# Kernel tuning notes

Measured on AMD Instinct MI355X. Metric: run time of the kernel, lower is better.

## Reference

```python
import jax, jax.numpy as jnp
import numpy as np

# FP4 E2M1 lookup: low 3 bits -> magnitude {0,.5,1,1.5,2,3,4,6}, bit 3 -> sign
FP4_LUT = jnp.array([0.0, 0.5, 1.0, 1.5, 2.0, 3.0, 4.0, 6.0,
                     -0.0, -0.5, -1.0, -1.5, -2.0, -3.0, -4.0, -6.0], dtype=jnp.float32)


def _dequant(packed_i32, scales, group_size):
    """packed_i32: [K/8, N] (8 FP4 nibbles per word along K); scales: [K/group_size, N] fp16.
    Returns dense [K, N] float32 weight."""
    p = packed_i32.astype(jnp.uint32)
    shifts = (jnp.arange(8, dtype=jnp.uint32) * jnp.uint32(4))
    nib = ((p[:, None, :] >> shifts[None, :, None]) & jnp.uint32(0xF)).astype(jnp.int32)  # [K/8,8,N]
    K = p.shape[0] * 8
    vals = FP4_LUT[nib.reshape(K, p.shape[1])]  # [K, N] f32
    g = jnp.arange(K) // group_size
    return vals * scales.astype(jnp.float32)[g]


def setup_inputs() -> dict:
    key = jax.random.key(0)
    k1, k2, k3, k4, k5 = jax.random.split(key, 5)
    B, H, I, G = 32, 4096, 2048, 128
    x = (jax.random.normal(k1, (B, H), dtype=jnp.float32) * 0.5).astype(jnp.float16)
    gate_up_packed = jax.random.bits(k2, (H // 8, 2 * I), dtype=jnp.uint32).astype(jnp.int32)
    down_packed = jax.random.bits(k3, (I // 8, H), dtype=jnp.uint32).astype(jnp.int32)
    gate_up_scales = (jax.random.uniform(k4, (H // G, 2 * I), minval=0.005, maxval=0.02)).astype(jnp.float16)
    down_scales = (jax.random.uniform(k5, (I // G, H), minval=0.005, maxval=0.02)).astype(jnp.float16)
    return {"x": x, "gate_up_packed": gate_up_packed, "gate_up_scales": gate_up_scales,
            "down_packed": down_packed, "down_scales": down_scales, "group_size": G}


def reference(x, gate_up_packed, gate_up_scales, down_packed, down_scales, group_size):
    w_gu = _dequant(gate_up_packed, gate_up_scales, group_size)   # [H, 2I]
    h = jnp.einsum('bh,hn->bn', x.astype(jnp.float32), w_gu)      # [B, 2I]
    inter = h.shape[1] // 2
    act = jax.nn.silu(h[:, :inter]) * h[:, inter:]                # SwiGLU
    w_d = _dequant(down_packed, down_scales, group_size)          # [I, H]
    out = jnp.einsum('bi,ih->bh', act, w_d)
    return out.astype(jnp.float16)
```

## Files before the change

kernel.cpp:

```cpp
#include <hip/hip_runtime.h>
#include <cstdint>

typedef float f32x4 __attribute__((ext_vector_type(4)));

constexpr int Bv = 32;
constexpr int Hv = 4096;
constexpr int Iv = 2048;
constexpr int N1 = 4096;

__device__ __forceinline__ long dec8(uint32_t w) {
  uint32_t lo = w & 0x07070707u;
  uint32_t hi = (w >> 4) & 0x07070707u;
  uint32_t me = __builtin_amdgcn_perm(0x4C484440u, 0x3C383000u, lo);
  uint32_t mo = __builtin_amdgcn_perm(0x4C484440u, 0x3C383000u, hi);
  uint32_t e  = me | ((w & 0x08080808u) << 4);
  uint32_t o  = mo | (w & 0x80808080u);
  uint32_t d0 = __builtin_amdgcn_perm(o, e, 0x05010400u);
  uint32_t d1 = __builtin_amdgcn_perm(o, e, 0x07030602u);
  return (long)(((uint64_t)d1 << 32) | d0);
}

__global__ __launch_bounds__(256) void k_prep(const float* __restrict__ x,
                                              uint32_t* __restrict__ xh,
                                              uint32_t* __restrict__ xl) {
  const int t = blockIdx.x * 256 + threadIdx.x;
  const float* p = x + t * 8;
  f32x4 v0 = *(const f32x4*)p;
  f32x4 v1 = *(const f32x4*)(p + 4);
  float f[8] = {v0[0], v0[1], v0[2], v0[3], v1[0], v1[1], v1[2], v1[3]};
  uint32_t h0 = 0, h1 = 0;
  h0 = __builtin_amdgcn_cvt_pk_fp8_f32(f[0], f[1], h0, false);
  h0 = __builtin_amdgcn_cvt_pk_fp8_f32(f[2], f[3], h0, true);
  h1 = __builtin_amdgcn_cvt_pk_fp8_f32(f[4], f[5], h1, false);
  h1 = __builtin_amdgcn_cvt_pk_fp8_f32(f[6], f[7], h1, true);
  float r[8];
  r[0] = f[0] - __builtin_amdgcn_cvt_f32_fp8(h0, 0);
  r[1] = f[1] - __builtin_amdgcn_cvt_f32_fp8(h0, 1);
  r[2] = f[2] - __builtin_amdgcn_cvt_f32_fp8(h0, 2);
  r[3] = f[3] - __builtin_amdgcn_cvt_f32_fp8(h0, 3);
  r[4] = f[4] - __builtin_amdgcn_cvt_f32_fp8(h1, 0);
  r[5] = f[5] - __builtin_amdgcn_cvt_f32_fp8(h1, 1);
  r[6] = f[6] - __builtin_amdgcn_cvt_f32_fp8(h1, 2);
  r[7] = f[7] - __builtin_amdgcn_cvt_f32_fp8(h1, 3);
  uint32_t l0 = 0, l1 = 0;
  l0 = __builtin_amdgcn_cvt_pk_fp8_f32(r[0], r[1], l0, false);
  l0 = __builtin_amdgcn_cvt_pk_fp8_f32(r[2], r[3], l0, true);
  l1 = __builtin_amdgcn_cvt_pk_fp8_f32(r[4], r[5], l1, false);
  l1 = __builtin_amdgcn_cvt_pk_fp8_f32(r[6], r[7], l1, true);
  xh[t*2] = h0; xh[t*2+1] = h1;
  xl[t*2] = l0; xl[t*2+1] = l1;
}

__global__ __launch_bounds__(1024, 4) void k_gateup(
    const uint8_t* __restrict__ xh, const uint8_t* __restrict__ xl,
    const uint32_t* __restrict__ wp, const float* __restrict__ sc,
    float* __restrict__ hp) {
  __shared__ float lds[16 * 1024];
  const int nt = blockIdx.x >> 1;
  const int kh = blockIdx.x & 1;
  const int wid = threadIdx.x >> 6, lane = threadIdx.x & 63;
  const int q = lane >> 4, r = lane & 15;
  const int n0 = nt * 32;
  const int nA = n0 + r, nB = n0 + 16 + r;

  const int koff = kh * 2048 + wid * 128 + q * 8;
  const uint8_t* pa0h = xh + r * Hv + koff;
  const uint8_t* pa0l = xl + r * Hv + koff;
  const uint8_t* pa1h = xh + (r + 16) * Hv + koff;
  const uint8_t* pa1l = xl + (r + 16) * Hv + koff;
  const uint32_t* pbA = wp + (size_t)(kh * 256 + wid * 16 + q) * N1 + nA;
  const uint32_t* pbB = pbA + 16;

  f32x4 t00 = {0,0,0,0}, t01 = {0,0,0,0}, t10 = {0,0,0,0}, t11 = {0,0,0,0};
  #pragma unroll
  for (int st = 0; st < 4; ++st) {
    long A0h = *(const long*)(pa0h + st * 32);
    long A0l = *(const long*)(pa0l + st * 32);
    long A1h = *(const long*)(pa1h + st * 32);
    long A1l = *(const long*)(pa1l + st * 32);
    long BA = dec8(pbA[(size_t)st * 4 * N1]);
    long BB = dec8(pbB[(size_t)st * 4 * N1]);
    t00 = __builtin_amdgcn_mfma_f32_16x16x32_fp8_fp8(A0h, BA, t00, 0, 0, 0);
    t00 = __builtin_amdgcn_mfma_f32_16x16x32_fp8_fp8(A0l, BA, t00, 0, 0, 0);
    t01 = __builtin_amdgcn_mfma_f32_16x16x32_fp8_fp8(A0h, BB, t01, 0, 0, 0);
    t01 = __builtin_amdgcn_mfma_f32_16x16x32_fp8_fp8(A0l, BB, t01, 0, 0, 0);
    t10 = __builtin_amdgcn_mfma_f32_16x16x32_fp8_fp8(A1h, BA, t10, 0, 0, 0);
    t10 = __builtin_amdgcn_mfma_f32_16x16x32_fp8_fp8(A1l, BA, t10, 0, 0, 0);
    t11 = __builtin_amdgcn_mfma_f32_16x16x32_fp8_fp8(A1h, BB, t11, 0, 0, 0);
    t11 = __builtin_amdgcn_mfma_f32_16x16x32_fp8_fp8(A1l, BB, t11, 0, 0, 0);
  }
  const int g = kh * 16 + wid;
  const float sA = sc[g * N1 + nA];
  const float sB = sc[g * N1 + nB];
  float* my = lds + wid * 1024;
  #pragma unroll
  for (int j = 0; j < 4; ++j) {
    const int rw = q * 4 + j;
    my[rw * 32 + r]             = sA * t00[j];
    my[rw * 32 + 16 + r]        = sB * t01[j];
    my[(16 + rw) * 32 + r]      = sA * t10[j];
    my[(16 + rw) * 32 + 16 + r] = sB * t11[j];
  }
  __syncthreads();
  const int i = threadIdx.x;
  float sum = 0.f;
  #pragma unroll
  for (int w = 0; w < 16; ++w) sum += lds[w * 1024 + i];
  hp[(size_t)kh * (Bv * N1) + (i >> 5) * N1 + n0 + (i & 31)] = sum;
}

__global__ __launch_bounds__(256) void k_swiglu(const float* __restrict__ hp,
                                                uint32_t* __restrict__ ah,
                                                uint32_t* __restrict__ al) {
  const int t = blockIdx.x * 256 + threadIdx.x;
  const int m = t >> 9;
  const int c = (t & 511) * 4;
  constexpr int P = Bv * N1;
  const float* pg = hp + m * N1 + c;
  const float* pu = pg + Iv;
  f32x4 g = *(const f32x4*)pg + *(const f32x4*)(pg + P);
  f32x4 u = *(const f32x4*)pu + *(const f32x4*)(pu + P);
  float a[4];
  #pragma unroll
  for (int j = 0; j < 4; ++j) {
    float gv = g[j];
    float av = gv / (1.0f + __expf(-gv)) * u[j];
    a[j] = fminf(fmaxf(av, -440.0f), 440.0f);
  }
  uint32_t h = 0;
  h = __builtin_amdgcn_cvt_pk_fp8_f32(a[0], a[1], h, false);
  h = __builtin_amdgcn_cvt_pk_fp8_f32(a[2], a[3], h, true);
  float r0 = a[0] - __builtin_amdgcn_cvt_f32_fp8(h, 0);
  float r1 = a[1] - __builtin_amdgcn_cvt_f32_fp8(h, 1);
  float r2 = a[2] - __builtin_amdgcn_cvt_f32_fp8(h, 2);
  float r3 = a[3] - __builtin_amdgcn_cvt_f32_fp8(h, 3);
  uint32_t l = 0;
  l = __builtin_amdgcn_cvt_pk_fp8_f32(r0, r1, l, false);
  l = __builtin_amdgcn_cvt_pk_fp8_f32(r2, r3, l, true);
  ah[t] = h; al[t] = l;
}

__global__ __launch_bounds__(1024, 4) void k_down(
    const uint8_t* __restrict__ ah8, const uint8_t* __restrict__ al8,
    const uint32_t* __restrict__ wp, const float* __restrict__ sc,
    float* __restrict__ out) {
  __shared__ float lds[16 * 512];
  const int n0 = blockIdx.x * 16;
  const int wid = threadIdx.x >> 6, lane = threadIdx.x & 63;
  const int q = lane >> 4, r = lane & 15;
  const int n = n0 + r;

  const int koff = wid * 128 + q * 8;
  const uint8_t* pa0h = ah8 + r * Iv + koff;
  const uint8_t* pa0l = al8 + r * Iv + koff;
  const uint8_t* pa1h = ah8 + (r + 16) * Iv + koff;
  const uint8_t* pa1l = al8 + (r + 16) * Iv + koff;
  const uint32_t* pb = wp + (size_t)(wid * 16 + q) * Hv + n;

  f32x4 t0 = {0,0,0,0}, t1 = {0,0,0,0};
  #pragma unroll
  for (int st = 0; st < 4; ++st) {
    long A0h = *(const long*)(pa0h + st * 32);
    long A0l = *(const long*)(pa0l + st * 32);
    long A1h = *(const long*)(pa1h + st * 32);
    long A1l = *(const long*)(pa1l + st * 32);
    long Bf = dec8(pb[(size_t)st * 4 * Hv]);
    t0 = __builtin_amdgcn_mfma_f32_16x16x32_fp8_fp8(A0h, Bf, t0, 0, 0, 0);
    t0 = __builtin_amdgcn_mfma_f32_16x16x32_fp8_fp8(A0l, Bf, t0, 0, 0, 0);
    t1 = __builtin_amdgcn_mfma_f32_16x16x32_fp8_fp8(A1h, Bf, t1, 0, 0, 0);
    t1 = __builtin_amdgcn_mfma_f32_16x16x32_fp8_fp8(A1l, Bf, t1, 0, 0, 0);
  }
  const float sv = sc[wid * Hv + n];
  float* my = lds + wid * 512;
  #pragma unroll
  for (int j = 0; j < 4; ++j) {
    const int rw = q * 4 + j;
    my[rw * 16 + r]        = sv * t0[j];
    my[(16 + rw) * 16 + r] = sv * t1[j];
  }
  __syncthreads();
  const int i = threadIdx.x;
  if (i < 512) {
    float sum = 0.f;
    #pragma unroll
    for (int w = 0; w < 16; ++w) sum += lds[w * 512 + i];
    out[(i >> 4) * N1 + n0 + (i & 15)] = sum;
  }
}

extern "C" void kernel_launch(void* const* d_in, const int* in_sizes, int n_in,
                              void* d_out, int out_size, void* d_ws, size_t ws_size,
                              hipStream_t stream) {
  const float*    x   = (const float*)d_in[0];
  const uint32_t* gup = (const uint32_t*)d_in[1];
  const float*    gus = (const float*)d_in[2];
  const uint32_t* dnp = (const uint32_t*)d_in[3];
  const float*    dns = (const float*)d_in[4];

  float*    hpart = (float*)d_ws;
  uint8_t*  xh    = (uint8_t*)d_ws + 2*(size_t)Bv*N1*sizeof(float);
  uint8_t*  xl    = xh + Bv*Hv;
  uint8_t*  a8h   = xl + Bv*Hv;
  uint8_t*  a8l   = a8h + Bv*Iv;

  k_prep  <<< 64,  256, 0, stream>>>(x, (uint32_t*)xh, (uint32_t*)xl);
  k_gateup<<<256, 1024, 0, stream>>>(xh, xl, gup, gus, hpart);
  k_swiglu<<< 64,  256, 0, stream>>>(hpart, (uint32_t*)a8h, (uint32_t*)a8l);
  k_down  <<<256, 1024, 0, stream>>>(a8h, a8l, dnp, dns, (float*)d_out);
}
```

Measured before the change: 93.35 us.

## Fuse SwiGLU into gate/up GEMM by pairing gate and up columns per block

Each gate/up block now computes the matching 16 gate and 16 up columns over the full K range. Every wave covers two scale groups and does the SwiGLU activation plus the fp8 hi/lo split directly from the LDS reduction. This removes the separate swiglu kernel, the fp32 partial-sum round trip through global memory and the K-split. In exchange the grid drops from 256 to 128 blocks, each wave does twice the sequential work, and the activation outputs are written as single bytes instead of packed words.

```diff
diff --git a/kernel.cpp b/kernel.cpp
--- a/kernel.cpp
+++ b/kernel.cpp
@@ -51,93 +51,89 @@
   xl[t*2] = l0; xl[t*2+1] = l1;
 }
 
-__global__ __launch_bounds__(1024, 4) void k_gateup(
+__global__ __launch_bounds__(1024, 4) void k_fused(
     const uint8_t* __restrict__ xh, const uint8_t* __restrict__ xl,
     const uint32_t* __restrict__ wp, const float* __restrict__ sc,
-    float* __restrict__ hp) {
-  __shared__ float lds[16 * 1024];
-  const int nt = blockIdx.x >> 1;
-  const int kh = blockIdx.x & 1;
+    uint8_t* __restrict__ a8h, uint8_t* __restrict__ a8l) {
+  __shared__ float ldsg[16 * 512];
+  __shared__ float ldsu[16 * 512];
+  const int c0 = blockIdx.x * 16;
   const int wid = threadIdx.x >> 6, lane = threadIdx.x & 63;
   const int q = lane >> 4, r = lane & 15;
-  const int n0 = nt * 32;
-  const int nA = n0 + r, nB = n0 + 16 + r;
-
-  const int koff = kh * 2048 + wid * 128 + q * 8;
+  const int ng = c0 + r;
+  const int nu = Iv + c0 + r;
+
+  const int koff = wid * 256 + q * 8;
   const uint8_t* pa0h = xh + r * Hv + koff;
   const uint8_t* pa0l = xl + r * Hv + koff;
   const uint8_t* pa1h = xh + (r + 16) * Hv + koff;
   const uint8_t* pa1l = xl + (r + 16) * Hv + koff;
-  const uint32_t* pbA = wp + (size_t)(kh * 256 + wid * 16 + q) * N1 + nA;
-  const uint32_t* pbB = pbA + 16;
-
-  f32x4 t00 = {0,0,0,0}, t01 = {0,0,0,0}, t10 = {0,0,0,0}, t11 = {0,0,0,0};
-  #pragma unroll
-  for (int st = 0; st < 4; ++st) {
-    long A0h = *(const long*)(pa0h + st * 32);
-    long A0l = *(const long*)(pa0l + st * 32);
-    long A1h = *(const long*)(pa1h + st * 32);
-    long A1l = *(const long*)(pa1l + st * 32);
-    long BA = dec8(pbA[(size_t)st * 4 * N1]);
-    long BB = dec8(pbB[(size_t)st * 4 * N1]);
-    t00 = __builtin_amdgcn_mfma_f32_16x16x32_fp8_fp8(A0h, BA, t00, 0, 0, 0);
-    t00 = __builtin_amdgcn_mfma_f32_16x16x32_fp8_fp8(A0l, BA, t00, 0, 0, 0);
-    t01 = __builtin_amdgcn_mfma_f32_16x16x32_fp8_fp8(A0h, BB, t01, 0, 0, 0);
-    t01 = __builtin_amdgcn_mfma_f32_16x16x32_fp8_fp8(A0l, BB, t01, 0, 0, 0);
-    t10 = __builtin_amdgcn_mfma_f32_16x16x32_fp8_fp8(A1h, BA, t10, 0, 0, 0);
-    t10 = __builtin_amdgcn_mfma_f32_16x16x32_fp8_fp8(A1l, BA, t10, 0, 0, 0);
-    t11 = __builtin_amdgcn_mfma_f32_16x16x32_fp8_fp8(A1h, BB, t11, 0, 0, 0);
-    t11 = __builtin_amdgcn_mfma_f32_16x16x32_fp8_fp8(A1l, BB, t11, 0, 0, 0);
-  }
-  const int g = kh * 16 + wid;
-  const float sA = sc[g * N1 + nA];
-  const float sB = sc[g * N1 + nB];
-  float* my = lds + wid * 1024;
+  const uint32_t* pbg = wp + (size_t)(wid * 32 + q) * N1 + ng;
+  const uint32_t* pbu = wp + (size_t)(wid * 32 + q) * N1 + nu;
+
+  f32x4 ag0 = {0,0,0,0}, ag1 = {0,0,0,0}, au0 = {0,0,0,0}, au1 = {0,0,0,0};
+
+  #pragma unroll
+  for (int g = 0; g < 2; ++g) {
+    f32x4 tg0 = {0,0,0,0}, tg1 = {0,0,0,0}, tu0 = {0,0,0,0}, tu1 = {0,0,0,0};
+    #pragma unroll
+    for (int st = 0; st < 4; ++st) {
+      const int ke = g * 128 + st * 32;
+      const size_t kw = (size_t)(g * 16 + st * 4) * N1;
+      long A0h = *(const long*)(pa0h + ke);
+      long A0l = *(const long*)(pa0l + ke);
+      long A1h = *(const long*)(pa1h + ke);
+      long A1l = *(const long*)(pa1l + ke);
+      long Bg = dec8(pbg[kw]);
+      long Bu = dec8(pbu[kw]);
+      tg0 = __builtin_amdgcn_mfma_f32_16x16x32_fp8_fp8(A0h, Bg, tg0, 0, 0, 0);
+      tg0 = __builtin_amdgcn_mfma_f32_16x16x32_fp8_fp8(A0l, Bg, tg0, 0, 0, 0);
+      tg1 = __builtin_amdgcn_mfma_f32_16x16x32_fp8_fp8(A1h, Bg, tg1, 0, 0, 0);
+      tg1 = __builtin_amdgcn_mfma_f32_16x16x32_fp8_fp8(A1l, Bg, tg1, 0, 0, 0);
+      tu0 = __builtin_amdgcn_mfma_f32_16x16x32_fp8_fp8(A0h, Bu, tu0, 0, 0, 0);
+      tu0 = __builtin_amdgcn_mfma_f32_16x16x32_fp8_fp8(A0l, Bu, tu0, 0, 0, 0);
+      tu1 = __builtin_amdgcn_mfma_f32_16x16x32_fp8_fp8(A1h, Bu, tu1, 0, 0, 0);
+      tu1 = __builtin_amdgcn_mfma_f32_16x16x32_fp8_fp8(A1l, Bu, tu1, 0, 0, 0);
+    }
+    const int grp = wid * 2 + g;
+    const float sg = sc[grp * N1 + ng];
+    const float su = sc[grp * N1 + nu];
+    #pragma unroll
+    for (int j = 0; j < 4; ++j) {
+      ag0[j] = fmaf(sg, tg0[j], ag0[j]);
+      ag1[j] = fmaf(sg, tg1[j], ag1[j]);
+      au0[j] = fmaf(su, tu0[j], au0[j]);
+      au1[j] = fmaf(su, tu1[j], au1[j]);
+    }
+  }
+  float* mg = ldsg + wid * 512;
+  float* mu = ldsu + wid * 512;
   #pragma unroll
   for (int j = 0; j < 4; ++j) {
     const int rw = q * 4 + j;
-    my[rw * 32 + r]             = sA * t00[j];
-    my[rw * 32 + 16 + r]        = sB * t01[j];
-    my[(16 + rw) * 32 + r]      = sA * t10[j];
-    my[(16 + rw) * 32 + 16 + r] = sB * t11[j];
+    mg[rw * 16 + r]        = ag0[j];
+    mg[(16 + rw) * 16 + r] = ag1[j];
+    mu[rw * 16 + r]        = au0[j];
+    mu[(16 + rw) * 16 + r] = au1[j];
   }
   __syncthreads();
   const int i = threadIdx.x;
-  float sum = 0.f;
-  #pragma unroll
-  for (int w = 0; w < 16; ++w) sum += lds[w * 1024 + i];
-  hp[(size_t)kh * (Bv * N1) + (i >> 5) * N1 + n0 + (i & 31)] = sum;
-}
-
-__global__ __launch_bounds__(256) void k_swiglu(const float* __restrict__ hp,
-                                                uint32_t* __restrict__ ah,
-                                                uint32_t* __restrict__ al) {
-  const int t = blockIdx.x * 256 + threadIdx.x;
-  const int m = t >> 9;
-  const int c = (t & 511) * 4;
-  constexpr int P = Bv * N1;
-  const float* pg = hp + m * N1 + c;
-  const float* pu = pg + Iv;
-  f32x4 g = *(const f32x4*)pg + *(const f32x4*)(pg + P);
-  f32x4 u = *(const f32x4*)pu + *(const f32x4*)(pu + P);
-  float a[4];
-  #pragma unroll
-  for (int j = 0; j < 4; ++j) {
-    float gv = g[j];
-    float av = gv / (1.0f + __expf(-gv)) * u[j];
-    a[j] = fminf(fmaxf(av, -440.0f), 440.0f);
-  }
-  uint32_t h = 0;
-  h = __builtin_amdgcn_cvt_pk_fp8_f32(a[0], a[1], h, false);
-  h = __builtin_amdgcn_cvt_pk_fp8_f32(a[2], a[3], h, true);
-  float r0 = a[0] - __builtin_amdgcn_cvt_f32_fp8(h, 0);
-  float r1 = a[1] - __builtin_amdgcn_cvt_f32_fp8(h, 1);
-  float r2 = a[2] - __builtin_amdgcn_cvt_f32_fp8(h, 2);
-  float r3 = a[3] - __builtin_amdgcn_cvt_f32_fp8(h, 3);
-  uint32_t l = 0;
-  l = __builtin_amdgcn_cvt_pk_fp8_f32(r0, r1, l, false);
-  l = __builtin_amdgcn_cvt_pk_fp8_f32(r2, r3, l, true);
-  ah[t] = h; al[t] = l;
+  if (i < 512) {
+    float gv = 0.f, uv = 0.f;
+    #pragma unroll
+    for (int w = 0; w < 16; ++w) {
+      gv += ldsg[w * 512 + i];
+      uv += ldsu[w * 512 + i];
+    }
+    float av = gv / (1.0f + __expf(-gv)) * uv;
+    av = fminf(fmaxf(av, -440.0f), 440.0f);
+    uint32_t hb = __builtin_amdgcn_cvt_pk_fp8_f32(av, av, 0, false);
+    float rv = av - __builtin_amdgcn_cvt_f32_fp8(hb, 0);
+    uint32_t lb = __builtin_amdgcn_cvt_pk_fp8_f32(rv, rv, 0, false);
+    const int off = (i >> 4) * Iv + c0 + (i & 15);
+    a8h[off] = (uint8_t)(hb & 0xFF);
+    a8l[off] = (uint8_t)(lb & 0xFF);
+  }
 }
 
 __global__ __launch_bounds__(1024, 4) void k_down(
@@ -197,14 +193,12 @@
   const uint32_t* dnp = (const uint32_t*)d_in[3];
   const float*    dns = (const float*)d_in[4];
 
-  float*    hpart = (float*)d_ws;
-  uint8_t*  xh    = (uint8_t*)d_ws + 2*(size_t)Bv*N1*sizeof(float);
-  uint8_t*  xl    = xh + Bv*Hv;
-  uint8_t*  a8h   = xl + Bv*Hv;
-  uint8_t*  a8l   = a8h + Bv*Iv;
-
-  k_prep  <<< 64,  256, 0, stream>>>(x, (uint32_t*)xh, (uint32_t*)xl);
-  k_gateup<<<256, 1024, 0, stream>>>(xh, xl, gup, gus, hpart);
-  k_swiglu<<< 64,  256, 0, stream>>>(hpart, (uint32_t*)a8h, (uint32_t*)a8l);
-  k_down  <<<256, 1024, 0, stream>>>(a8h, a8l, dnp, dns, (float*)d_out);
-}
+  uint8_t*  xh  = (uint8_t*)d_ws;
+  uint8_t*  xl  = xh + Bv*Hv;
+  uint8_t*  a8h = xl + Bv*Hv;
+  uint8_t*  a8l = a8h + Bv*Iv;
+
+  k_prep <<< 64,  256, 0, stream>>>(x, (uint32_t*)xh, (uint32_t*)xl);
+  k_fused<<<128, 1024, 0, stream>>>(xh, xl, gup, gus, a8h, a8l);
+  k_down <<<256, 1024, 0, stream>>>(a8h, a8l, dnp, dns, (float*)d_out);
+}
```

Result: slower. 99.67 us (+6.8%).
